# Kernel tuning notes

Measured on AMD Instinct MI355X. Metric: run time of the kernel, lower is better.

The kernel has to match this reference:

```python
import jax, jax.numpy as jnp
import numpy as np

D_MODEL = 1024
NUM_HEADS = 16
D_K = D_MODEL // NUM_HEADS
B, S = 2, 2048


def setup_inputs() -> dict:
    key = jax.random.key(0)
    ks = jax.random.split(key, 4)
    scale = 1.0 / np.sqrt(D_MODEL)
    x = jax.random.normal(ks[0], (B, S, D_MODEL), dtype=jnp.float32)
    w_qkv = jax.random.normal(ks[1], (D_MODEL, 3 * D_MODEL), dtype=jnp.float32) * scale
    b_qkv = jnp.zeros((3 * D_MODEL,), dtype=jnp.float32)
    w_out = jax.random.normal(ks[2], (D_MODEL, D_MODEL), dtype=jnp.float32) * scale
    b_out = jnp.zeros((D_MODEL,), dtype=jnp.float32)
    # causal mask: 1 where attention is allowed (j <= i), 0 elsewhere
    mask = jnp.tril(jnp.ones((S, S), dtype=jnp.int32))
    return {"x": x, "mask": mask, "w_qkv": w_qkv, "b_qkv": b_qkv,
            "w_out": w_out, "b_out": b_out}


def reference(x, mask, w_qkv, b_qkv, w_out, b_out):
    Bb, Ss, C = x.shape
    qkv = x @ w_qkv + b_qkv                      # [B,S,3C]
    q, k, v = jnp.split(qkv, 3, axis=-1)
    def split_heads(t):
        return t.reshape(Bb, Ss, NUM_HEADS, D_K).transpose(0, 2, 1, 3)  # [B,H,S,Dk]
    q, k, v = split_heads(q), split_heads(k), split_heads(v)
    scores = jnp.einsum('bhqd,bhkd->bhqk', q, k) / jnp.sqrt(jnp.float32(D_K))
    scores = jnp.where(mask == 0, -jnp.inf, scores)
    weights = jax.nn.softmax(scores, axis=-1)
    weights = jnp.nan_to_num(weights, nan=0.0)   # matches torch.nan_to_num
    attn = jnp.einsum('bhqk,bhkd->bhqd', weights, v)
    attn = attn.transpose(0, 2, 1, 3).reshape(Bb, Ss, C)
    return attn @ w_out + b_out
```

## Files before the change

### kernel.cpp

```cpp
#include <hip/hip_runtime.h>
#include <hip/hip_bf16.h>

#define D_MODEL 1024
#define NUM_HEADS 16
#define D_K 64
#define BATCH 2
#define SEQ 2048

typedef __attribute__((ext_vector_type(8))) short bf16x8;
typedef __attribute__((ext_vector_type(4))) float f32x4;

union P16 { int4 i4; ushort u[8]; };
union FU { float f; unsigned int u; };

__device__ __forceinline__ float bf2f(ushort u) {
    union { unsigned int i; float f; } c; c.i = ((unsigned int)u) << 16; return c.f;
}
__device__ __forceinline__ ushort f2bf(float f) {
    union { float f; unsigned int i; } c; c.f = f;
    unsigned int x = c.i;
    return (ushort)((x + 0x7fff + ((x >> 16) & 1)) >> 16);
}
__device__ __forceinline__ unsigned int cvt_pk_bf16(float lo, float hi) {
    unsigned int r;
    asm("v_cvt_pk_bf16_f32 %0, %1, %2" : "=v"(r) : "v"(lo), "v"(hi));
    return r;
}
__device__ __forceinline__ void gll16(const void* g, void* l) {
    __builtin_amdgcn_global_load_lds(
        (const __attribute__((address_space(1))) void*)g,
        (__attribute__((address_space(3))) void*)l,
        16, 0, 0);
}

__device__ __forceinline__ bool wave_detect_f32(const ushort* x) {
    ushort u = x[2 * (threadIdx.x & 63)];
    int e = (u >> 7) & 0xFF;
    unsigned long long bl = __ballot(e >= 100 && e <= 141);
    return __popcll(bl) < 32;
}

__global__ __launch_bounds__(256)
void prep_all(const ushort* __restrict__ x, const void* __restrict__ Wq,
              const void* __restrict__ Wo, ushort* __restrict__ xb,
              ushort* __restrict__ WqT, ushort* __restrict__ WoT,
              int* __restrict__ flag)
{
    const bool f32 = wave_detect_f32(x);
    const int bx = blockIdx.x, tx = threadIdx.x;
    if (bx == 0 && tx == 0) flag[0] = f32 ? 1 : 0;

    if (bx >= 1024) {
        if (!f32) return;
        int i = ((bx - 1024) * 256 + tx) * 8;
        const float* f = (const float*)x + i;
        float4 a = *(const float4*)f, b = *(const float4*)(f + 4);
        P16 r;
        r.u[0] = f2bf(a.x); r.u[1] = f2bf(a.y); r.u[2] = f2bf(a.z); r.u[3] = f2bf(a.w);
        r.u[4] = f2bf(b.x); r.u[5] = f2bf(b.y); r.u[6] = f2bf(b.z); r.u[7] = f2bf(b.w);
        *(int4*)(xb + i) = r.i4;
        return;
    }

    __shared__ ushort t[64][72];
    const int nb = bx & 63, kb = bx >> 6;
    const void* W; ushort* WT; int N, n0;
    if (nb < 48) { W = Wq; WT = WqT; N = 3 * D_MODEL; n0 = nb * 64; }
    else         { W = Wo; WT = WoT; N = D_MODEL;     n0 = (nb - 48) * 64; }
    const int k0 = kb * 64, K = D_MODEL;
    #pragma unroll
    for (int p = 0; p < 16; ++p) {
        int r = p * 4 + (tx >> 6), c = tx & 63;
        float v = f32 ? ((const float*)W)[(size_t)(k0 + r) * N + n0 + c]
                      : bf2f(((const ushort*)W)[(size_t)(k0 + r) * N + n0 + c]);
        t[r][c] = f2bf(v);
    }
    __syncthreads();
    #pragma unroll
    for (int p = 0; p < 16; ++p) {
        int nn = p * 4 + (tx >> 6), kk = tx & 63;
        WT[(size_t)(n0 + nn) * K + k0 + kk] = t[kk][nn];
    }
}

template<int MODE>
__global__ __launch_bounds__(256)
void gemm128(const void* __restrict__ Araw, const ushort* __restrict__ Aconv,
             const ushort* __restrict__ WT, const void* __restrict__ bias,
             void* __restrict__ out, int N, int K, const int* __restrict__ flag)
{
    __shared__ ushort As[2][128 * 32];
    __shared__ ushort Bs[2][128 * 32];

    const int f = *flag;
    const ushort* A = (MODE == 1) ? (f ? Aconv : (const ushort*)Araw) : Aconv;

    const int tid = threadIdx.x;
    const int w = tid >> 6, lane = tid & 63;
    const int ln = lane & 15, quad = lane >> 4;
    const int m0 = blockIdx.y * 128, n0 = blockIdx.x * 128;
    const int wm = (w >> 1) * 64, wn = (w & 1) * 64;

    const int s0 = w * 128 + lane, s1 = s0 + 64;
    const int ar0 = s0 >> 2, ak0 = ((s0 & 3) ^ ((ar0 >> 1) & 3)) * 8;
    const int ar1 = s1 >> 2, ak1 = ((s1 & 3) ^ ((ar1 >> 1) & 3)) * 8;
    const size_t aoff0 = (size_t)(m0 + ar0) * K + ak0;
    const size_t aoff1 = (size_t)(m0 + ar1) * K + ak1;
    const size_t boff0 = (size_t)(n0 + ar0) * K + ak0;
    const size_t boff1 = (size_t)(n0 + ar1) * K + ak1;

    const int physc = (quad ^ ((ln >> 1) & 3)) * 8;

    f32x4 acc[4][4] = {};

    const int nk = K >> 5;
    gll16(A + aoff0,  As[0] + s0 * 8);
    gll16(A + aoff1,  As[0] + s1 * 8);
    gll16(WT + boff0, Bs[0] + s0 * 8);
    gll16(WT + boff1, Bs[0] + s1 * 8);
    __syncthreads();

    for (int kt = 0; kt < nk; ++kt) {
        const int cur = kt & 1;
        if (kt + 1 < nk) {
            const int kc = (kt + 1) * 32;
            gll16(A + aoff0 + kc,  As[1 - cur] + s0 * 8);
            gll16(A + aoff1 + kc,  As[1 - cur] + s1 * 8);
            gll16(WT + boff0 + kc, Bs[1 - cur] + s0 * 8);
            gll16(WT + boff1 + kc, Bs[1 - cur] + s1 * 8);
        }

        bf16x8 af[4], bf[4];
        #pragma unroll
        for (int t = 0; t < 4; ++t) {
            af[t] = *(const bf16x8*)(As[cur] + (wm + t * 16 + ln) * 32 + physc);
            bf[t] = *(const bf16x8*)(Bs[cur] + (wn + t * 16 + ln) * 32 + physc);
        }
        #pragma unroll
        for (int mi = 0; mi < 4; ++mi)
            #pragma unroll
            for (int ni = 0; ni < 4; ++ni)
                acc[mi][ni] = __builtin_amdgcn_mfma_f32_16x16x32_bf16(
                    af[mi], bf[ni], acc[mi][ni], 0, 0, 0);
        __syncthreads();
    }

    #pragma unroll
    for (int mi = 0; mi < 4; ++mi) {
        #pragma unroll
        for (int ni = 0; ni < 4; ++ni) {
            int col = n0 + wn + ni * 16 + ln;
            float bb = f ? ((const float*)bias)[col] : bf2f(((const ushort*)bias)[col]);
            #pragma unroll
            for (int r = 0; r < 4; ++r) {
                int row = m0 + wm + mi * 16 + quad * 4 + r;
                float v = acc[mi][ni][r] + bb;
                if (MODE == 0 && f) ((float*)out)[(size_t)row * N + col] = v;
                else                ((ushort*)out)[(size_t)row * N + col] = f2bf(v);
            }
        }
    }
}

template<int MODE>
__global__ __launch_bounds__(256)
void gemm64(const void* __restrict__ Araw, const ushort* __restrict__ Aconv,
            const ushort* __restrict__ WT, const void* __restrict__ bias,
            void* __restrict__ out, int N, int K, const int* __restrict__ flag)
{
    __shared__ ushort As[2][64 * 32];
    __shared__ ushort Bs[2][128 * 32];

    const int f = *flag;
    const ushort* A = (MODE == 1) ? (f ? Aconv : (const ushort*)Araw) : Aconv;

    const int tid = threadIdx.x;
    const int w = tid >> 6, lane = tid & 63;
    const int ln = lane & 15, quad = lane >> 4;
    const int m0 = blockIdx.y * 64, n0 = blockIdx.x * 128;
    const int wn = w * 32;

    const int sa = tid;
    const int arow = sa >> 2, akc = ((sa & 3) ^ ((arow >> 1) & 3)) * 8;
    const size_t aoff = (size_t)(m0 + arow) * K + akc;
    const int sb0 = tid, sb1 = tid + 256;
    const int br0 = sb0 >> 2, bk0 = ((sb0 & 3) ^ ((br0 >> 1) & 3)) * 8;
    const int br1 = sb1 >> 2, bk1 = ((sb1 & 3) ^ ((br1 >> 1) & 3)) * 8;
    const size_t boff0 = (size_t)(n0 + br0) * K + bk0;
    const size_t boff1 = (size_t)(n0 + br1) * K + bk1;

    const int physc = (quad ^ ((ln >> 1) & 3)) * 8;

    f32x4 acc[4][2] = {};

    const int nk = K >> 5;
    gll16(A + aoff,   As[0] + sa * 8);
    gll16(WT + boff0, Bs[0] + sb0 * 8);
    gll16(WT + boff1, Bs[0] + sb1 * 8);
    __syncthreads();

    for (int kt = 0; kt < nk; ++kt) {
        const int cur = kt & 1;
        if (kt + 1 < nk) {
            const int kc = (kt + 1) * 32;
            gll16(A + aoff + kc,   As[1 - cur] + sa * 8);
            gll16(WT + boff0 + kc, Bs[1 - cur] + sb0 * 8);
            gll16(WT + boff1 + kc, Bs[1 - cur] + sb1 * 8);
        }

        bf16x8 af[4], bf[2];
        #pragma unroll
        for (int t = 0; t < 4; ++t)
            af[t] = *(const bf16x8*)(As[cur] + (t * 16 + ln) * 32 + physc);
        #pragma unroll
        for (int t = 0; t < 2; ++t)
            bf[t] = *(const bf16x8*)(Bs[cur] + (wn + t * 16 + ln) * 32 + physc);
        #pragma unroll
        for (int mi = 0; mi < 4; ++mi)
            #pragma unroll
            for (int ni = 0; ni < 2; ++ni)
                acc[mi][ni] = __builtin_amdgcn_mfma_f32_16x16x32_bf16(
                    af[mi], bf[ni], acc[mi][ni], 0, 0, 0);
        __syncthreads();
    }

    #pragma unroll
    for (int mi = 0; mi < 4; ++mi) {
        #pragma unroll
        for (int ni = 0; ni < 2; ++ni) {
            int col = n0 + wn + ni * 16 + ln;
            float bb = f ? ((const float*)bias)[col] : bf2f(((const ushort*)bias)[col]);
            #pragma unroll
            for (int r = 0; r < 4; ++r) {
                int row = m0 + mi * 16 + quad * 4 + r;
                float v = acc[mi][ni][r] + bb;
                if (MODE == 0 && f) ((float*)out)[(size_t)row * N + col] = v;
                else                ((ushort*)out)[(size_t)row * N + col] = f2bf(v);
            }
        }
    }
}

__global__ __launch_bounds__(256)
void flash_attn13(const ushort* __restrict__ qkv, ushort* __restrict__ attn)
{
    __shared__ ushort Ks[64][72];
    __shared__ ushort Vs[64][72];
    __shared__ ushort QPs[128][72];

    const int tid  = threadIdx.x;
    const int wave = tid >> 6, lane = tid & 63;
    const int ln   = lane & 15, quad = lane >> 4;
    const int pg   = wave >> 1, ww = wave & 1;
    const int bh   = blockIdx.x;
    const int ky   = blockIdx.y;
    const int k    = (ky < 8) ? ky : 23 - ky;
    const int xx   = 2 * k + pg;
    const int b    = bh >> 4, hh = bh & (NUM_HEADS - 1);
    const int W3   = 3 * D_MODEL;
    const size_t hbase = (size_t)b * SEQ * W3 + hh * D_K;

    const int q0A = 32 * (63 - xx), q0B = 32 * xx;
    const int ntA = 32 - k, ntB = k + 1;

    const int qrr = tid >> 1, qcol = (tid & 1) * 32;
    const int ksr = tid >> 2, ksc = (tid & 3) * 16;
    const int vp  = tid & 31, vg = (tid >> 5) * 8;

    const int vkey = 2 * vp;
    const int vcol = (vkey & 32) + ((vkey >> 2) & 3) * 8 + ((vkey >> 4) & 1) * 4 + (vkey & 3);

    {
        const int qpg = qrr >> 6, qmt = (qrr >> 5) & 1, ql = qrr & 31;
        const int qxx = 2 * k + qpg;
        const int grow = qmt ? (32 * qxx + ql) : (32 * (63 - qxx) + ql);
        const ushort* src = qkv + hbase + (size_t)grow * W3 + qcol;
        #pragma unroll
        for (int h = 0; h < 4; ++h) {
            P16 v; v.i4 = *(const int4*)(src + h * 8);
            #pragma unroll
            for (int e = 0; e < 8; ++e) v.u[e] = f2bf(bf2f(v.u[e]) * 0.18033688011f);
            *(int4*)(&QPs[qrr][qcol + h * 8]) = v.i4;
        }
    }
    __syncthreads();
    bf16x8 qf[2][2];
    #pragma unroll
    for (int mt = 0; mt < 2; ++mt)
        #pragma unroll
        for (int s = 0; s < 2; ++s)
            qf[mt][s] = *(const bf16x8*)(&QPs[pg * 64 + mt * 32 + ww * 16 + ln][s * 32 + quad * 8]);

    f32x4 acc_o[2][4] = {};
    f32x4 acc_l[2] = {};

    bf16x8 ones8;
    #pragma unroll
    for (int e = 0; e < 8; ++e) ones8[e] = (short)0x3F80;

    const ushort* Kbase = qkv + hbase + D_MODEL;
    const ushort* Vbase = qkv + hbase + 2 * D_MODEL;

    int4 kreg[2], vreg[2];
    {
        const ushort* ksrc = Kbase + (size_t)ksr * W3 + ksc;
        kreg[0] = *(const int4*)(ksrc);
        kreg[1] = *(const int4*)(ksrc + 8);
        vreg[0] = *(const int4*)(Vbase + (size_t)(2 * vp)     * W3 + vg);
        vreg[1] = *(const int4*)(Vbase + (size_t)(2 * vp + 1) * W3 + vg);
    }

    for (int jt = 0; jt < ntA; ++jt) {
        const int j0 = jt * 64;
        const bool doB = (jt < ntB);
        __syncthreads();

        *(int4*)(&Ks[ksr][ksc])     = kreg[0];
        *(int4*)(&Ks[ksr][ksc + 8]) = kreg[1];
        {
            P16 v0, v1; v0.i4 = vreg[0]; v1.i4 = vreg[1];
            #pragma unroll
            for (int e = 0; e < 8; ++e) {
                unsigned int pack = (unsigned int)v0.u[e] | ((unsigned int)v1.u[e] << 16);
                *(unsigned int*)(&Vs[vg + e][vcol]) = pack;
            }
        }
        __syncthreads();

        if (jt + 1 < ntA) {
            const int jn = j0 + 64;
            const ushort* ksrc = Kbase + (size_t)(jn + ksr) * W3 + ksc;
            kreg[0] = *(const int4*)(ksrc);
            kreg[1] = *(const int4*)(ksrc + 8);
            vreg[0] = *(const int4*)(Vbase + (size_t)(jn + 2 * vp)     * W3 + vg);
            vreg[1] = *(const int4*)(Vbase + (size_t)(jn + 2 * vp + 1) * W3 + vg);
        }

        f32x4 sa[2][4];
        #pragma unroll
        for (int t = 0; t < 4; ++t) {
            bf16x8 k0 = *(const bf16x8*)(&Ks[t * 16 + ln][quad * 8]);
            bf16x8 k1 = *(const bf16x8*)(&Ks[t * 16 + ln][32 + quad * 8]);
            {
                f32x4 z = {};
                z = __builtin_amdgcn_mfma_f32_16x16x32_bf16(k0, qf[0][0], z, 0, 0, 0);
                z = __builtin_amdgcn_mfma_f32_16x16x32_bf16(k1, qf[0][1], z, 0, 0, 0);
                sa[0][t] = z;
            }
            if (doB) {
                f32x4 z = {};
                z = __builtin_amdgcn_mfma_f32_16x16x32_bf16(k0, qf[1][0], z, 0, 0, 0);
                z = __builtin_amdgcn_mfma_f32_16x16x32_bf16(k1, qf[1][1], z, 0, 0, 0);
                sa[1][t] = z;
            }
        }

        if (jt == ntA - 1) {
            const int qrow = q0A + ww * 16 + ln;
            #pragma unroll
            for (int t = 0; t < 4; ++t)
                #pragma unroll
                for (int r = 0; r < 4; ++r)
                    if (j0 + t * 16 + quad * 4 + r > qrow) sa[0][t][r] = -1e30f;
        }
        if (doB && jt == ntB - 1) {
            const int qrow = q0B + ww * 16 + ln;
            #pragma unroll
            for (int t = 0; t < 4; ++t)
                #pragma unroll
                for (int r = 0; r < 4; ++r)
                    if (j0 + t * 16 + quad * 4 + r > qrow) sa[1][t][r] = -1e30f;
        }

        union PB { unsigned int w[4]; bf16x8 v; };
        PB pa[2][2];
        #pragma unroll
        for (int mt = 0; mt < 2; ++mt) {
            if (mt && !doB) break;
            #pragma unroll
            for (int s = 0; s < 2; ++s) {
                #pragma unroll
                for (int w = 0; w < 4; ++w) {
                    const int t = 2 * s + (w >> 1);
                    const int r0 = (w & 1) * 2;
                    float lo = __builtin_amdgcn_exp2f(sa[mt][t][r0]);
                    float hi = __builtin_amdgcn_exp2f(sa[mt][t][r0 + 1]);
                    pa[mt][s].w[w] = cvt_pk_bf16(lo, hi);
                }
            }
        }

        #pragma unroll
        for (int s = 0; s < 2; ++s) {
            #pragma unroll
            for (int t = 0; t < 4; ++t) {
                bf16x8 vf = *(const bf16x8*)(&Vs[t * 16 + ln][s * 32 + quad * 8]);
                acc_o[0][t] = __builtin_amdgcn_mfma_f32_16x16x32_bf16(pa[0][s].v, vf, acc_o[0][t], 0, 0, 0);
                if (doB)
                    acc_o[1][t] = __builtin_amdgcn_mfma_f32_16x16x32_bf16(pa[1][s].v, vf, acc_o[1][t], 0, 0, 0);
            }
            acc_l[0] = __builtin_amdgcn_mfma_f32_16x16x32_bf16(pa[0][s].v, ones8, acc_l[0], 0, 0, 0);
            if (doB)
                acc_l[1] = __builtin_amdgcn_mfma_f32_16x16x32_bf16(pa[1][s].v, ones8, acc_l[1], 0, 0, 0);
        }
    }

    #pragma unroll
    for (int mt = 0; mt < 2; ++mt) {
        const int q0 = mt ? q0B : q0A;
        #pragma unroll
        for (int r = 0; r < 4; ++r) {
            float inv = 1.0f / acc_l[mt][r];
            int i = q0 + ww * 16 + quad * 4 + r;
            size_t rowoff = ((size_t)(b * SEQ + i)) * D_MODEL + hh * D_K;
            #pragma unroll
            for (int t = 0; t < 4; ++t)
                attn[rowoff + t * 16 + ln] = f2bf(acc_o[mt][t][r] * inv);
        }
    }
}

extern "C" void kernel_launch(void* const* d_in, const int* in_sizes, int n_in,
                              void* d_out, int out_size, void* d_ws, size_t ws_size,
                              hipStream_t stream)
{
    const void* x     = d_in[0];
    const void* w_qkv = d_in[2];
    const void* b_qkv = d_in[3];
    const void* w_out = d_in[4];
    const void* b_out = d_in[5];

    char* ws = (char*)d_ws;
    int*    flag   = (int*)ws;                  size_t off = 256;
    ushort* WqkvT  = (ushort*)(ws + off);       off += (size_t)3 * D_MODEL * D_MODEL * 2;
    ushort* WoutT  = (ushort*)(ws + off);       off += (size_t)D_MODEL * D_MODEL * 2;
    ushort* qkv_ws = (ushort*)(ws + off);       off += (size_t)BATCH * SEQ * 3 * D_MODEL * 2;
    ushort* xb     = (ushort*)(ws + off);
    ushort* attn_ws = xb;

    const int M = BATCH * SEQ;

    prep_all<<<3072, 256, 0, stream>>>((const ushort*)x, w_qkv, w_out,
                                       xb, WqkvT, WoutT, flag);

    gemm128<1><<<dim3(3 * D_MODEL / 128, M / 128), 256, 0, stream>>>(
        x, xb, WqkvT, b_qkv, qkv_ws, 3 * D_MODEL, D_MODEL, flag);

    dim3 ga(BATCH * NUM_HEADS, 16);
    flash_attn13<<<ga, 256, 0, stream>>>(qkv_ws, attn_ws);

    gemm64<0><<<dim3(D_MODEL / 128, M / 64), 256, 0, stream>>>(
        attn_ws, attn_ws, WoutT, b_out, d_out, D_MODEL, D_MODEL, flag);
}
```

Measured before the change: 210.2 us.

## Split attention KV loop across two blocks and combine partial outputs

Adds a split-KV flash attention kernel where each query tile pair is processed by two blocks handling alternating key tiles. Each block writes unnormalized fp32 partial outputs and row sums, and a new combine kernel sums the halves, normalizes and converts to bf16. This doubles the grid to improve occupancy and parallelism across the many compute units. In exchange it adds fp32 partial-output traffic and an extra kernel launch. The old path remains as a fallback when the workspace is too small.

```diff
diff --git a/kernel.cpp b/kernel.cpp
--- a/kernel.cpp
+++ b/kernel.cpp
@@ -239,6 +239,221 @@
             }
         }
     }
+}
+
+__global__ __launch_bounds__(256)
+void flash_attn15(const ushort* __restrict__ qkv, float* __restrict__ pO,
+                  float* __restrict__ pL)
+{
+    __shared__ ushort Ks[64][72];
+    __shared__ ushort Vs[64][72];
+
+    const int tid  = threadIdx.x;
+    const int wave = tid >> 6, lane = tid & 63;
+    const int ln   = lane & 15, quad = lane >> 4;
+    const int pg   = wave >> 1, ww = wave & 1;
+    const int bh   = blockIdx.x;
+    const int yy   = blockIdx.y;
+    const int ky   = yy >> 1, half = yy & 1;
+    const int k    = (ky < 8) ? ky : 23 - ky;
+    const int xx   = 2 * k + pg;
+    const int b    = bh >> 4, hh = bh & (NUM_HEADS - 1);
+    const int W3   = 3 * D_MODEL;
+    const size_t hbase = (size_t)b * SEQ * W3 + hh * D_K;
+
+    const int q0A = 32 * (63 - xx), q0B = 32 * xx;
+    const int ntA = 32 - k, ntB = k + 1;
+
+    const int qrr = tid >> 1, qcol = (tid & 1) * 32;
+    const int ksr = tid >> 2, ksc = (tid & 3) * 16;
+    const int vp  = tid & 31, vg = (tid >> 5) * 8;
+
+    const int vkey = 2 * vp;
+    const int vcol = (vkey & 32) + ((vkey >> 2) & 3) * 8 + ((vkey >> 4) & 1) * 4 + (vkey & 3);
+
+    {
+        const int qpg = qrr >> 6, qmt = (qrr >> 5) & 1, ql = qrr & 31;
+        const int qxx = 2 * k + qpg;
+        const int grow = qmt ? (32 * qxx + ql) : (32 * (63 - qxx) + ql);
+        const ushort* src = qkv + hbase + (size_t)grow * W3 + qcol;
+        ushort* dst = (qrr < 64) ? &Ks[qrr][qcol] : &Vs[qrr - 64][qcol];
+        #pragma unroll
+        for (int h = 0; h < 4; ++h) {
+            P16 v; v.i4 = *(const int4*)(src + h * 8);
+            #pragma unroll
+            for (int e = 0; e < 8; ++e) v.u[e] = f2bf(bf2f(v.u[e]) * 0.18033688011f);
+            *(int4*)(dst + h * 8) = v.i4;
+        }
+    }
+    __syncthreads();
+    bf16x8 qf[2][2];
+    {
+        const ushort (*Qarr)[72] = pg ? Vs : Ks;
+        #pragma unroll
+        for (int mt = 0; mt < 2; ++mt)
+            #pragma unroll
+            for (int s = 0; s < 2; ++s)
+                qf[mt][s] = *(const bf16x8*)(&Qarr[mt * 32 + ww * 16 + ln][s * 32 + quad * 8]);
+    }
+
+    f32x4 acc_o[2][4] = {};
+    f32x4 acc_l[2] = {};
+
+    bf16x8 ones8;
+    #pragma unroll
+    for (int e = 0; e < 8; ++e) ones8[e] = (short)0x3F80;
+
+    const ushort* Kbase = qkv + hbase + D_MODEL;
+    const ushort* Vbase = qkv + hbase + 2 * D_MODEL;
+
+    int4 kreg[2], vreg[2];
+    {
+        const int jf = half * 64;
+        const ushort* ksrc = Kbase + (size_t)(jf + ksr) * W3 + ksc;
+        kreg[0] = *(const int4*)(ksrc);
+        kreg[1] = *(const int4*)(ksrc + 8);
+        vreg[0] = *(const int4*)(Vbase + (size_t)(jf + 2 * vp)     * W3 + vg);
+        vreg[1] = *(const int4*)(Vbase + (size_t)(jf + 2 * vp + 1) * W3 + vg);
+    }
+
+    for (int jt = half; jt < ntA; jt += 2) {
+        const int j0 = jt * 64;
+        const bool doB = (jt < ntB);
+        __syncthreads();
+
+        *(int4*)(&Ks[ksr][ksc])     = kreg[0];
+        *(int4*)(&Ks[ksr][ksc + 8]) = kreg[1];
+        {
+            P16 v0, v1; v0.i4 = vreg[0]; v1.i4 = vreg[1];
+            #pragma unroll
+            for (int e = 0; e < 8; ++e) {
+                unsigned int pack = (unsigned int)v0.u[e] | ((unsigned int)v1.u[e] << 16);
+                *(unsigned int*)(&Vs[vg + e][vcol]) = pack;
+            }
+        }
+        __syncthreads();
+
+        if (jt + 2 < ntA) {
+            const int jn = j0 + 128;
+            const ushort* ksrc = Kbase + (size_t)(jn + ksr) * W3 + ksc;
+            kreg[0] = *(const int4*)(ksrc);
+            kreg[1] = *(const int4*)(ksrc + 8);
+            vreg[0] = *(const int4*)(Vbase + (size_t)(jn + 2 * vp)     * W3 + vg);
+            vreg[1] = *(const int4*)(Vbase + (size_t)(jn + 2 * vp + 1) * W3 + vg);
+        }
+
+        f32x4 sa[2][4];
+        #pragma unroll
+        for (int t = 0; t < 4; ++t) {
+            bf16x8 k0 = *(const bf16x8*)(&Ks[t * 16 + ln][quad * 8]);
+            bf16x8 k1 = *(const bf16x8*)(&Ks[t * 16 + ln][32 + quad * 8]);
+            {
+                f32x4 z = {};
+                z = __builtin_amdgcn_mfma_f32_16x16x32_bf16(k0, qf[0][0], z, 0, 0, 0);
+                z = __builtin_amdgcn_mfma_f32_16x16x32_bf16(k1, qf[0][1], z, 0, 0, 0);
+                sa[0][t] = z;
+            }
+            if (doB) {
+                f32x4 z = {};
+                z = __builtin_amdgcn_mfma_f32_16x16x32_bf16(k0, qf[1][0], z, 0, 0, 0);
+                z = __builtin_amdgcn_mfma_f32_16x16x32_bf16(k1, qf[1][1], z, 0, 0, 0);
+                sa[1][t] = z;
+            }
+        }
+
+        if (jt == ntA - 1) {
+            const int qrow = q0A + ww * 16 + ln;
+            #pragma unroll
+            for (int t = 0; t < 4; ++t)
+                #pragma unroll
+                for (int r = 0; r < 4; ++r)
+                    if (j0 + t * 16 + quad * 4 + r > qrow) sa[0][t][r] = -1e30f;
+        }
+        if (doB && jt == ntB - 1) {
+            const int qrow = q0B + ww * 16 + ln;
+            #pragma unroll
+            for (int t = 0; t < 4; ++t)
+                #pragma unroll
+                for (int r = 0; r < 4; ++r)
+                    if (j0 + t * 16 + quad * 4 + r > qrow) sa[1][t][r] = -1e30f;
+        }
+
+        union PB { unsigned int w[4]; bf16x8 v; };
+        PB pa[2][2];
+        #pragma unroll
+        for (int mt = 0; mt < 2; ++mt) {
+            if (mt && !doB) break;
+            #pragma unroll
+            for (int s = 0; s < 2; ++s) {
+                #pragma unroll
+                for (int w = 0; w < 4; ++w) {
+                    const int t = 2 * s + (w >> 1);
+                    const int r0 = (w & 1) * 2;
+                    float lo = __builtin_amdgcn_exp2f(sa[mt][t][r0]);
+                    float hi = __builtin_amdgcn_exp2f(sa[mt][t][r0 + 1]);
+                    pa[mt][s].w[w] = cvt_pk_bf16(lo, hi);
+                }
+            }
+        }
+
+        #pragma unroll
+        for (int s = 0; s < 2; ++s) {
+            #pragma unroll
+            for (int t = 0; t < 4; ++t) {
+                bf16x8 vf = *(const bf16x8*)(&Vs[t * 16 + ln][s * 32 + quad * 8]);
+                acc_o[0][t] = __builtin_amdgcn_mfma_f32_16x16x32_bf16(pa[0][s].v, vf, acc_o[0][t], 0, 0, 0);
+                if (doB)
+                    acc_o[1][t] = __builtin_amdgcn_mfma_f32_16x16x32_bf16(pa[1][s].v, vf, acc_o[1][t], 0, 0, 0);
+            }
+            acc_l[0] = __builtin_amdgcn_mfma_f32_16x16x32_bf16(pa[0][s].v, ones8, acc_l[0], 0, 0, 0);
+            if (doB)
+                acc_l[1] = __builtin_amdgcn_mfma_f32_16x16x32_bf16(pa[1][s].v, ones8, acc_l[1], 0, 0, 0);
+        }
+    }
+
+    const size_t oH = (size_t)half * BATCH * SEQ * D_MODEL;
+    const size_t lH = (size_t)half * BATCH * SEQ * NUM_HEADS;
+    #pragma unroll
+    for (int mt = 0; mt < 2; ++mt) {
+        const int q0 = mt ? q0B : q0A;
+        #pragma unroll
+        for (int r = 0; r < 4; ++r) {
+            int i = q0 + ww * 16 + quad * 4 + r;
+            size_t rowoff = ((size_t)(b * SEQ + i)) * D_MODEL + hh * D_K;
+            #pragma unroll
+            for (int t = 0; t < 4; ++t)
+                pO[oH + rowoff + t * 16 + ln] = acc_o[mt][t][r];
+            if (ln == 0)
+                pL[lH + (size_t)(b * SEQ + i) * NUM_HEADS + hh] = acc_l[mt][r];
+        }
+    }
+}
+
+__global__ __launch_bounds__(256)
+void combine_halves(const float* __restrict__ pO, const float* __restrict__ pL,
+                    ushort* __restrict__ attn)
+{
+    constexpr size_t HALF_O = (size_t)BATCH * SEQ * D_MODEL;
+    constexpr size_t HALF_L = (size_t)BATCH * SEQ * NUM_HEADS;
+    const size_t idx = ((size_t)blockIdx.x * 256 + threadIdx.x) * 8;
+    const int row = (int)(idx >> 10);
+    const int hh  = (int)((idx >> 6) & 15);
+    const float il = 1.0f / (pL[(size_t)row * NUM_HEADS + hh] +
+                             pL[HALF_L + (size_t)row * NUM_HEADS + hh]);
+    float4 a0 = *(const float4*)(pO + idx);
+    float4 a1 = *(const float4*)(pO + idx + 4);
+    float4 b0 = *(const float4*)(pO + HALF_O + idx);
+    float4 b1 = *(const float4*)(pO + HALF_O + idx + 4);
+    P16 r;
+    r.u[0] = f2bf((a0.x + b0.x) * il);
+    r.u[1] = f2bf((a0.y + b0.y) * il);
+    r.u[2] = f2bf((a0.z + b0.z) * il);
+    r.u[3] = f2bf((a0.w + b0.w) * il);
+    r.u[4] = f2bf((a1.x + b1.x) * il);
+    r.u[5] = f2bf((a1.y + b1.y) * il);
+    r.u[6] = f2bf((a1.z + b1.z) * il);
+    r.u[7] = f2bf((a1.w + b1.w) * il);
+    *(int4*)(attn + idx) = r.i4;
 }
 
 __global__ __launch_bounds__(256)
@@ -435,8 +650,15 @@
     ushort* WqkvT  = (ushort*)(ws + off);       off += (size_t)3 * D_MODEL * D_MODEL * 2;
     ushort* WoutT  = (ushort*)(ws + off);       off += (size_t)D_MODEL * D_MODEL * 2;
     ushort* qkv_ws = (ushort*)(ws + off);       off += (size_t)BATCH * SEQ * 3 * D_MODEL * 2;
-    ushort* xb     = (ushort*)(ws + off);
-    ushort* attn_ws = xb;
+    char*   share  = ws + off;
+    ushort* xb     = (ushort*)share;
+    float*  pO     = (float*)share;
+    const size_t pO_bytes = (size_t)2 * BATCH * SEQ * D_MODEL * 4;
+    float*  pL     = (float*)(share + pO_bytes);
+    const size_t pL_bytes = (size_t)2 * BATCH * SEQ * NUM_HEADS * 4;
+    const bool use_split = ws_size >= off + pO_bytes + pL_bytes;
+    ushort* attn_split = qkv_ws;
+    ushort* attn_fb    = xb;
 
     const int M = BATCH * SEQ;
 
@@ -446,9 +668,17 @@
     gemm128<1><<<dim3(3 * D_MODEL / 128, M / 128), 256, 0, stream>>>(
         x, xb, WqkvT, b_qkv, qkv_ws, 3 * D_MODEL, D_MODEL, flag);
 
-    dim3 ga(BATCH * NUM_HEADS, 16);
-    flash_attn13<<<ga, 256, 0, stream>>>(qkv_ws, attn_ws);
-
-    gemm64<0><<<dim3(D_MODEL / 128, M / 64), 256, 0, stream>>>(
-        attn_ws, attn_ws, WoutT, b_out, d_out, D_MODEL, D_MODEL, flag);
-}
+    if (use_split) {
+        dim3 ga(BATCH * NUM_HEADS, 32);
+        flash_attn15<<<ga, 256, 0, stream>>>(qkv_ws, pO, pL);
+        combine_halves<<<(BATCH * SEQ * D_MODEL) / (256 * 8), 256, 0, stream>>>(
+            pO, pL, attn_split);
+        gemm64<0><<<dim3(D_MODEL / 128, M / 64), 256, 0, stream>>>(
+            attn_split, attn_split, WoutT, b_out, d_out, D_MODEL, D_MODEL, flag);
+    } else {
+        dim3 ga(BATCH * NUM_HEADS, 16);
+        flash_attn13<<<ga, 256, 0, stream>>>(qkv_ws, attn_fb);
+        gemm64<0><<<dim3(D_MODEL / 128, M / 64), 256, 0, stream>>>(
+            attn_fb, attn_fb, WoutT, b_out, d_out, D_MODEL, D_MODEL, flag);
+    }
+}
```

New measurement: 217.7 us. +3.6%, slower.
